# Kernel optimization log

Hardware: AMD Instinct MI355X
Metric: run time of the kernel (lower is better)

The kernel has to match this reference:

```python
import jax, jax.numpy as jnp
import numpy as np

NUM_HEADS = 8
DIM_HEAD = 40
SCALE = DIM_HEAD ** (-1.0 / 4.0)  # applied to q AND k, net 1/sqrt(dim_head)


def setup_inputs() -> dict:
    key = jax.random.key(0)
    ks = jax.random.split(key, 7)
    B, T, Dq = 16, 4096, 320
    S, Dc = 77, 768
    inner = NUM_HEADS * DIM_HEAD  # 320
    return {
        "x": jax.random.normal(ks[0], (B, T, Dq), jnp.float32),
        "context": jax.random.normal(ks[1], (B, S, Dc), jnp.float32),
        "Wq": jax.random.normal(ks[2], (Dq, inner), jnp.float32) * 0.02,
        "Wk": jax.random.normal(ks[3], (Dc, inner), jnp.float32) * 0.02,
        "Wv": jax.random.normal(ks[4], (Dc, inner), jnp.float32) * 0.02,
        "Wo": jax.random.normal(ks[5], (inner, Dq), jnp.float32) * 0.02,
        "bo": jnp.zeros((Dq,), jnp.float32),
    }


def reference(x, context, Wq, Wk, Wv, Wo, bo):
    B, T, _ = x.shape
    S = context.shape[1]
    H, C = NUM_HEADS, DIM_HEAD
    # projections; scale applied to q and k separately (dim_head^-1/4 each)
    q = (x @ Wq * SCALE).reshape(B, T, H, C)        # [B,T,H,C]
    k = (context @ Wk * SCALE).reshape(B, S, H, C)  # [B,S,H,C]
    v = (context @ Wv).reshape(B, S, H, C)          # [B,S,H,C]
    scores = jnp.einsum("bthc,bshc->bhts", q, k)    # [B,H,T,S]
    attn = jax.nn.softmax(scores, axis=-1)
    out = jnp.einsum("bhts,bshc->bthc", attn, v).reshape(B, T, H * C)
    return out @ Wo + bo
```

## Files before the change

kernel.cpp:

```cpp
#include <hip/hip_runtime.h>
#include <math.h>


#define NUM_HEADS 8
#define DIM_HEAD 40
#define INNER 320
#define DQ 320
#define DC 768
#define SEQ_T 4096
#define SEQ_S 77
#define BATCH 16
#define M_TOTAL (BATCH * SEQ_T)
#define MKV 1232
#define MKV_PAD 1280
#define SCALE 0.39763536438352531f

typedef __attribute__((ext_vector_type(8))) short short8;
typedef __attribute__((ext_vector_type(4))) float floatx4;

__device__ __forceinline__ unsigned short f2bf(float f) {
  unsigned u = __float_as_uint(f);
  u += 0x7FFFu + ((u >> 16) & 1u);
  return (unsigned short)(u >> 16);
}

#define CTXBLKS (MKV_PAD * DC / 8 / 256)
__global__ __launch_bounds__(256) void convert_ctx_kernel(
    const float* __restrict__ ctx, unsigned short* __restrict__ ctxb) {
  size_t t = (size_t)blockIdx.x * 256 + threadIdx.x;
  int row = (int)(t / (DC / 8)), col = (int)(t % (DC / 8)) * 8;
  int4 pk = make_int4(0, 0, 0, 0);
  if (row < MKV) {
    const float* p = &ctx[(size_t)row * DC + col];
    float4 a = *(const float4*)p, b = *(const float4*)(p + 4);
    pk.x = (int)(f2bf(a.x) | ((unsigned)f2bf(a.y) << 16));
    pk.y = (int)(f2bf(a.z) | ((unsigned)f2bf(a.w) << 16));
    pk.z = (int)(f2bf(b.x) | ((unsigned)f2bf(b.y) << 16));
    pk.w = (int)(f2bf(b.z) | ((unsigned)f2bf(b.w) << 16));
  }
  *(int4*)&ctxb[(size_t)row * DC + col] = pk;
}

__global__ __launch_bounds__(256) void transpose_w_kernel(
    const float* __restrict__ Wq, const float* __restrict__ Wo,
    const float* __restrict__ Wk, const float* __restrict__ Wv,
    unsigned short* __restrict__ WqT, unsigned short* __restrict__ WoT,
    unsigned short* __restrict__ WkvT) {
  const int z = blockIdx.z;
  const float* W; unsigned short* WT; int KD; float scl = 1.0f;
  if (z == 0)      { W = Wq; WT = WqT;  KD = 320; }
  else if (z == 1) { W = Wo; WT = WoT;  KD = 320; }
  else if (z == 2) { W = Wk; WT = WkvT; KD = DC; scl = SCALE; }
  else             { W = Wv; WT = WkvT + (size_t)INNER * DC; KD = DC; }
  const int k0 = blockIdx.x * 32;
  if (k0 >= KD) return;
  const int n0 = blockIdx.y * 32;
  __shared__ float tile[32][33];
  int tx = threadIdx.x & 31, ty = threadIdx.x >> 5;
  #pragma unroll
  for (int r = 0; r < 4; ++r)
    tile[ty + r * 8][tx] = W[(size_t)(k0 + ty + r * 8) * 320 + n0 + tx];
  __syncthreads();
  #pragma unroll
  for (int r = 0; r < 4; ++r)
    WT[(size_t)(n0 + ty + r * 8) * KD + k0 + tx] = f2bf(tile[tx][ty + r * 8] * scl);
}

#define GBM 128
#define GBN 160
#define GBK 64

template <bool OUT_BF16, int K, int CN>
__global__ __launch_bounds__(256) void gemm_mfma_kernel(
    const unsigned short* __restrict__ A, const unsigned short* __restrict__ B,
    void* __restrict__ C, const float* __restrict__ bias, float scale) {
  __shared__ __align__(16) unsigned short As[GBM * GBK];
  __shared__ __align__(16) unsigned short Bs[GBN * GBK];
  const int tid = threadIdx.x;
  const int lane = tid & 63, wave = tid >> 6;
  const int wm = (wave & 1) * 64, wn = (wave >> 1) * 80;
  const int lrow = lane & 15, quad = lane >> 4;
  const unsigned short* Ab = A + (size_t)blockIdx.x * GBM * K;
  const unsigned short* Bb = B + (size_t)blockIdx.y * GBN * K;

  floatx4 acc[4][5];
  #pragma unroll
  for (int i = 0; i < 4; ++i)
    #pragma unroll
    for (int j = 0; j < 5; ++j) acc[i][j] = (floatx4){0.f, 0.f, 0.f, 0.f};

  for (int kb = 0; kb < K / GBK; ++kb) {
    const int k0 = kb * GBK;
    #pragma unroll
    for (int rnd = 0; rnd < 4; ++rnd) {
      int off = rnd * 4096 + tid * 16;
      int m = off >> 7, cl = (off >> 4) & 7, cg = cl ^ (m & 7);
      __builtin_amdgcn_global_load_lds(
          (const __attribute__((address_space(1))) void*)(Ab + (size_t)m * K + k0 + cg * 8),
          (__attribute__((address_space(3))) void*)((char*)As + off), 16, 0, 0);
    }
    #pragma unroll
    for (int rnd = 0; rnd < 5; ++rnd) {
      int off = rnd * 4096 + tid * 16;
      int n = off >> 7, cl = (off >> 4) & 7, cg = cl ^ (n & 7);
      __builtin_amdgcn_global_load_lds(
          (const __attribute__((address_space(1))) void*)(Bb + (size_t)n * K + k0 + cg * 8),
          (__attribute__((address_space(3))) void*)((char*)Bs + off), 16, 0, 0);
    }
    __syncthreads();
    #pragma unroll
    for (int ks = 0; ks < 2; ++ks) {
      short8 fa[4], fb[5];
      #pragma unroll
      for (int i = 0; i < 4; ++i) {
        int m = wm + i * 16 + lrow;
        int cl = (ks * 4 + quad) ^ (m & 7);
        fa[i] = *(const short8*)&As[m * GBK + cl * 8];
      }
      #pragma unroll
      for (int j = 0; j < 5; ++j) {
        int n = wn + j * 16 + lrow;
        int cl = (ks * 4 + quad) ^ (n & 7);
        fb[j] = *(const short8*)&Bs[n * GBK + cl * 8];
      }
      #pragma unroll
      for (int i = 0; i < 4; ++i)
        #pragma unroll
        for (int j = 0; j < 5; ++j)
          acc[i][j] = __builtin_amdgcn_mfma_f32_16x16x32_bf16(fa[i], fb[j], acc[i][j], 0, 0, 0);
    }
    __syncthreads();
  }
  #pragma unroll
  for (int i = 0; i < 4; ++i)
    #pragma unroll
    for (int j = 0; j < 5; ++j) {
      int n = blockIdx.y * GBN + wn + j * 16 + lrow;
      float bv = bias ? bias[n] : 0.f;
      #pragma unroll
      for (int r = 0; r < 4; ++r) {
        size_t m = (size_t)blockIdx.x * GBM + wm + i * 16 + quad * 4 + r;
        float val = acc[i][j][r] * scale + bv;
        if (OUT_BF16) ((unsigned short*)C)[m * CN + n] = f2bf(val);
        else          ((float*)C)[m * CN + n] = val;
      }
    }
}

template <bool OUT_BF16, bool A_FP32>
__global__ __launch_bounds__(256, 2) void gemm_wide_kernel(
    const void* __restrict__ Av, const unsigned short* __restrict__ B,
    void* __restrict__ C, const float* __restrict__ bias, float scale) {
  __shared__ __align__(16) unsigned short As[128 * 64];
  __shared__ __align__(16) unsigned short Bs[320 * 64];
  const int tid = threadIdx.x;
  const int lane = tid & 63, wave = tid >> 6;
  const int wm = (wave & 1) * 64, wn = (wave >> 1) * 160;
  const int lrow = lane & 15, quad = lane >> 4;

  floatx4 acc[4][10];
  #pragma unroll
  for (int i = 0; i < 4; ++i)
    #pragma unroll
    for (int j = 0; j < 10; ++j) acc[i][j] = (floatx4){0.f, 0.f, 0.f, 0.f};

  for (int kb = 0; kb < 5; ++kb) {
    const int k0 = kb * 64;
    if (A_FP32) {
      const float* Af = (const float*)Av + (size_t)blockIdx.x * 128 * 320;
      #pragma unroll
      for (int rnd = 0; rnd < 4; ++rnd) {
        int off = rnd * 4096 + tid * 16;
        int m = off >> 7, cl = (off >> 4) & 7, cg = cl ^ (m & 7);
        const float* src = Af + (size_t)m * 320 + k0 + cg * 8;
        float4 a = *(const float4*)src, b = *(const float4*)(src + 4);
        short8 pk;
        pk[0] = (short)f2bf(a.x); pk[1] = (short)f2bf(a.y);
        pk[2] = (short)f2bf(a.z); pk[3] = (short)f2bf(a.w);
        pk[4] = (short)f2bf(b.x); pk[5] = (short)f2bf(b.y);
        pk[6] = (short)f2bf(b.z); pk[7] = (short)f2bf(b.w);
        *(short8*)((char*)As + off) = pk;
      }
    } else {
      const unsigned short* Ab = (const unsigned short*)Av + (size_t)blockIdx.x * 128 * 320;
      #pragma unroll
      for (int rnd = 0; rnd < 4; ++rnd) {
        int off = rnd * 4096 + tid * 16;
        int m = off >> 7, cl = (off >> 4) & 7, cg = cl ^ (m & 7);
        __builtin_amdgcn_global_load_lds(
            (const __attribute__((address_space(1))) void*)(Ab + (size_t)m * 320 + k0 + cg * 8),
            (__attribute__((address_space(3))) void*)((char*)As + off), 16, 0, 0);
      }
    }
    #pragma unroll
    for (int rnd = 0; rnd < 10; ++rnd) {
      int off = rnd * 4096 + tid * 16;
      int n = off >> 7, cl = (off >> 4) & 7, cg = cl ^ (n & 7);
      __builtin_amdgcn_global_load_lds(
          (const __attribute__((address_space(1))) void*)(B + (size_t)n * 320 + k0 + cg * 8),
          (__attribute__((address_space(3))) void*)((char*)Bs + off), 16, 0, 0);
    }
    __syncthreads();
    #pragma unroll
    for (int ks = 0; ks < 2; ++ks) {
      short8 fa[4], fb[10];
      #pragma unroll
      for (int i = 0; i < 4; ++i) {
        int m = wm + i * 16 + lrow;
        int cl = (ks * 4 + quad) ^ (m & 7);
        fa[i] = *(const short8*)&As[m * 64 + cl * 8];
      }
      #pragma unroll
      for (int j = 0; j < 10; ++j) {
        int n = wn + j * 16 + lrow;
        int cl = (ks * 4 + quad) ^ (n & 7);
        fb[j] = *(const short8*)&Bs[n * 64 + cl * 8];
      }
      #pragma unroll
      for (int i = 0; i < 4; ++i)
        #pragma unroll
        for (int j = 0; j < 10; ++j)
          acc[i][j] = __builtin_amdgcn_mfma_f32_16x16x32_bf16(fa[i], fb[j], acc[i][j], 0, 0, 0);
    }
    __syncthreads();
  }
  #pragma unroll
  for (int i = 0; i < 4; ++i)
    #pragma unroll
    for (int j = 0; j < 10; ++j) {
      int n = wn + j * 16 + lrow;
      float bv = bias ? bias[n] : 0.f;
      #pragma unroll
      for (int r = 0; r < 4; ++r) {
        size_t m = (size_t)blockIdx.x * 128 + wm + i * 16 + quad * 4 + r;
        float val = acc[i][j][r] * scale + bv;
        if (OUT_BF16) ((unsigned short*)C)[m * 320 + n] = f2bf(val);
        else          ((float*)C)[m * 320 + n] = val;
      }
    }
}

__global__ __launch_bounds__(256) void attn_mfma_kernel(
    const unsigned short* __restrict__ q, const float* __restrict__ kv,
    unsigned short* __restrict__ o) {
  __shared__ __align__(16) unsigned short lds[24064];
  unsigned short* Kb = lds;
  unsigned short* Vt = lds + 5760;
  unsigned short* Qb = lds + 10752;
  const int tid = threadIdx.x;
  const int lane = tid & 63, wave = tid >> 6;
  const int lrow = lane & 15, quad = lane >> 4;
  unsigned short* Pw = lds + 10752 + wave * 3328;
  const int b = blockIdx.x >> 3, h = blockIdx.x & 7;
  const int t0 = blockIdx.y * 128;
  const unsigned short* qblk = q + ((size_t)b * SEQ_T + t0) * INNER + h * DIM_HEAD;

  #pragma unroll
  for (int rnd = 0; rnd < 3; ++rnd) {
    int off = rnd * 4096 + tid * 16;
    if (off < 10240) {
      int row = off / 80, rb = off % 80;
      __builtin_amdgcn_global_load_lds(
          (const __attribute__((address_space(1))) void*)(qblk + (size_t)row * INNER + rb / 2),
          (__attribute__((address_space(3))) void*)((char*)Qb + off), 16, 0, 0);
    }
  }
  {
    int4 z = make_int4(0, 0, 0, 0);
    for (int i = tid; i < 1344; i += 256) ((int4*)lds)[i] = z;
  }
  __syncthreads();

  const float* kvb = kv + (size_t)b * SEQ_S * 640;
  for (int idx = tid; idx < SEQ_S * 10; idx += 256) {
    int s = idx / 10, c4 = (idx % 10) * 4;
    float4 kx = *(const float4*)&kvb[s * 640 + h * DIM_HEAD + c4];
    float4 vx = *(const float4*)&kvb[s * 640 + 320 + h * DIM_HEAD + c4];
    *(ushort4*)&Kb[s * 72 + c4] =
        make_ushort4(f2bf(kx.x), f2bf(kx.y), f2bf(kx.z), f2bf(kx.w));
    Vt[(c4 + 0) * 104 + s] = f2bf(vx.x);
    Vt[(c4 + 1) * 104 + s] = f2bf(vx.y);
    Vt[(c4 + 2) * 104 + s] = f2bf(vx.z);
    Vt[(c4 + 3) * 104 + s] = f2bf(vx.w);
  }
  __syncthreads();

  short8 fa[2][2];
  const short8 zero8 = {0, 0, 0, 0, 0, 0, 0, 0};
  #pragma unroll
  for (int i = 0; i < 2; ++i) {
    int row = wave * 32 + i * 16 + lrow;
    fa[i][0] = *(const short8*)&Qb[row * 40 + quad * 8];
    fa[i][1] = (quad == 0) ? *(const short8*)&Qb[row * 40 + 32] : zero8;
  }
  __syncthreads();

  floatx4 sc[2][5];
  #pragma unroll
  for (int i = 0; i < 2; ++i)
    #pragma unroll
    for (int j = 0; j < 5; ++j) sc[i][j] = (floatx4){0.f, 0.f, 0.f, 0.f};
  #pragma unroll
  for (int j = 0; j < 5; ++j) {
    int srow = j * 16 + lrow;
    short8 fb0 = *(const short8*)&Kb[srow * 72 + quad * 8];
    short8 fb1 = *(const short8*)&Kb[srow * 72 + 32 + quad * 8];
    #pragma unroll
    for (int i = 0; i < 2; ++i) {
      sc[i][j] = __builtin_amdgcn_mfma_f32_16x16x32_bf16(fa[i][0], fb0, sc[i][j], 0, 0, 0);
      sc[i][j] = __builtin_amdgcn_mfma_f32_16x16x32_bf16(fa[i][1], fb1, sc[i][j], 0, 0, 0);
    }
  }

  float lsum[2][4];
  #pragma unroll
  for (int i = 0; i < 2; ++i)
    #pragma unroll
    for (int r = 0; r < 4; ++r) lsum[i][r] = 0.f;
  #pragma unroll
  for (int i = 0; i < 2; ++i) {
    #pragma unroll
    for (int j = 0; j < 5; ++j) {
      int s = j * 16 + lrow;
      #pragma unroll
      for (int r = 0; r < 4; ++r) {
        float p = (s < SEQ_S) ? __expf(sc[i][j][r]) : 0.f;
        Pw[(i * 16 + quad * 4 + r) * 104 + s] = f2bf(p);
        lsum[i][r] += p;
      }
    }
    #pragma unroll
    for (int r = 0; r < 4; ++r)
      Pw[(i * 16 + quad * 4 + r) * 104 + 80 + lrow] = 0;
  }
  #pragma unroll
  for (int i = 0; i < 2; ++i)
    #pragma unroll
    for (int r = 0; r < 4; ++r) {
      float v = lsum[i][r];
      v += __shfl_xor(v, 1); v += __shfl_xor(v, 2);
      v += __shfl_xor(v, 4); v += __shfl_xor(v, 8);
      lsum[i][r] = 1.0f / v;
    }

  floatx4 oc[2][3];
  #pragma unroll
  for (int i = 0; i < 2; ++i)
    #pragma unroll
    for (int nj = 0; nj < 3; ++nj) oc[i][nj] = (floatx4){0.f, 0.f, 0.f, 0.f};
  #pragma unroll
  for (int ks = 0; ks < 3; ++ks) {
    short8 pa[2];
    #pragma unroll
    for (int i = 0; i < 2; ++i)
      pa[i] = *(const short8*)&Pw[(i * 16 + lrow) * 104 + ks * 32 + quad * 8];
    #pragma unroll
    for (int nj = 0; nj < 3; ++nj) {
      short8 vb = *(const short8*)&Vt[(nj * 16 + lrow) * 104 + ks * 32 + quad * 8];
      #pragma unroll
      for (int i = 0; i < 2; ++i)
        oc[i][nj] = __builtin_amdgcn_mfma_f32_16x16x32_bf16(pa[i], vb, oc[i][nj], 0, 0, 0);
    }
  }

  __syncthreads();
  unsigned short* Ost = lds;
  #pragma unroll
  for (int i = 0; i < 2; ++i)
    #pragma unroll
    for (int nj = 0; nj < 3; ++nj) {
      int c = nj * 16 + lrow;
      if (c < DIM_HEAD) {
        #pragma unroll
        for (int r = 0; r < 4; ++r) {
          int row = wave * 32 + i * 16 + quad * 4 + r;
          Ost[row * 40 + c] = f2bf(oc[i][nj][r] * lsum[i][r]);
        }
      }
    }
  __syncthreads();
  unsigned short* oblk = o + ((size_t)b * SEQ_T + t0) * INNER + h * DIM_HEAD;
  for (int u = tid; u < 640; u += 256) {
    int row = u / 5, c8 = (u % 5) * 8;
    *(int4*)(oblk + (size_t)row * INNER + c8) = *(const int4*)&Ost[u * 8];
  }
}

extern "C" void kernel_launch(void* const* d_in, const int* in_sizes, int n_in,
                              void* d_out, int out_size, void* d_ws, size_t ws_size,
                              hipStream_t stream) {
  const float* x   = (const float*)d_in[0];
  const float* ctx = (const float*)d_in[1];
  const float* Wq  = (const float*)d_in[2];
  const float* Wk  = (const float*)d_in[3];
  const float* Wv  = (const float*)d_in[4];
  const float* Wo  = (const float*)d_in[5];
  const float* bo  = (const float*)d_in[6];
  float* out = (float*)d_out;

  char* w = (char*)d_ws;
  unsigned short* qo   = (unsigned short*)(w);
  unsigned short* ctxb = (unsigned short*)(w + 41943040);
  unsigned short* WkvT = (unsigned short*)(w + 43909120);
  float*          kvw  = (float*)(w + 44892160);
  unsigned short* WqT  = (unsigned short*)(w + 48168960);
  unsigned short* WoT  = (unsigned short*)(w + 48373760);

  hipLaunchKernelGGL(convert_ctx_kernel, dim3(CTXBLKS), dim3(256), 0, stream, ctx, ctxb);
  hipLaunchKernelGGL(transpose_w_kernel, dim3(24, 10, 4), dim3(256), 0, stream,
                     Wq, Wo, Wk, Wv, WqT, WoT, WkvT);
  hipLaunchKernelGGL((gemm_mfma_kernel<false, DC, 640>), dim3(MKV_PAD / GBM, 640 / GBN),
                     dim3(256), 0, stream, ctxb, WkvT, (void*)kvw, (const float*)nullptr, 1.0f);
  hipLaunchKernelGGL((gemm_wide_kernel<true, true>), dim3(M_TOTAL / 128), dim3(256), 0,
                     stream, (const void*)x, WqT, (void*)qo, (const float*)nullptr, SCALE);
  hipLaunchKernelGGL(attn_mfma_kernel, dim3(BATCH * NUM_HEADS, SEQ_T / 128), dim3(256), 0,
                     stream, qo, kvw, qo);
  hipLaunchKernelGGL((gemm_wide_kernel<false, false>), dim3(M_TOTAL / 128), dim3(256), 0,
                     stream, (const void*)qo, WoT, (void*)out, bo, 1.0f);
}
```

Measured before the change: 269.2 us.

## Fuse Q projection, attention and output projection into one kernel

Replaces the separate Q GEMM, attention kernel and output GEMM with a single 512-thread kernel per 128-row tile. The tile computes Q into LDS, loops over all 8 heads doing attention with K/V pre-converted to bf16 by a new prep kernel, and writes the result back into the same LDS buffer before running the Wo GEMM. This removes the bf16 Q and attention-output round trips through global memory and two launches. In exchange the kernel needs about 138KB of LDS, which limits it to one block per CU, and it serialises per-head syncs with fewer waves in flight.

Result: faster. 255.6 us (-5.1%).

```diff
diff --git a/kernel.cpp b/kernel.cpp
--- a/kernel.cpp
+++ b/kernel.cpp
@@ -147,242 +147,234 @@
     }
 }
 
-template <bool OUT_BF16, bool A_FP32>
-__global__ __launch_bounds__(256, 2) void gemm_wide_kernel(
-    const void* __restrict__ Av, const unsigned short* __restrict__ B,
-    void* __restrict__ C, const float* __restrict__ bias, float scale) {
-  __shared__ __align__(16) unsigned short As[128 * 64];
-  __shared__ __align__(16) unsigned short Bs[320 * 64];
+__global__ __launch_bounds__(256) void prep_kv_kernel(
+    const float* __restrict__ kvw, unsigned short* __restrict__ kvp) {
+  const int b = blockIdx.x >> 3, h = blockIdx.x & 7;
+  unsigned short* dst = kvp + (size_t)blockIdx.x * 8192;
+  const float* kvb = kvw + (size_t)b * SEQ_S * 640;
+  for (int i = threadIdx.x; i < 3200; i += 256) {
+    int s = i / 40, c = i % 40;
+    unsigned short v = 0;
+    if (s < SEQ_S) v = f2bf(kvb[(size_t)s * 640 + h * DIM_HEAD + c]);
+    dst[i] = v;
+  }
+  for (int i = threadIdx.x; i < 4992; i += 256) {
+    int c = i / 104, s = i % 104;
+    unsigned short v = 0;
+    if (s < SEQ_S && c < DIM_HEAD)
+      v = f2bf(kvb[(size_t)s * 640 + 320 + h * DIM_HEAD + c]);
+    dst[3200 + i] = v;
+  }
+}
+
+#define QS_STRIDE 328
+#define LDS_STAGE 41984
+
+__global__ __launch_bounds__(512) void fused_attn_kernel(
+    const float* __restrict__ x, const unsigned short* __restrict__ WqT,
+    const unsigned short* __restrict__ kvp, const unsigned short* __restrict__ WoT,
+    const float* __restrict__ bo, float* __restrict__ out) {
+  __shared__ __align__(16) unsigned short lds[70656];
+  unsigned short* qs = lds;
+  unsigned short* As = lds + LDS_STAGE;
+  unsigned short* Bs = lds + LDS_STAGE + 8192;
   const int tid = threadIdx.x;
   const int lane = tid & 63, wave = tid >> 6;
-  const int wm = (wave & 1) * 64, wn = (wave >> 1) * 160;
   const int lrow = lane & 15, quad = lane >> 4;
-
-  floatx4 acc[4][10];
-  #pragma unroll
-  for (int i = 0; i < 4; ++i)
-    #pragma unroll
-    for (int j = 0; j < 10; ++j) acc[i][j] = (floatx4){0.f, 0.f, 0.f, 0.f};
-
-  for (int kb = 0; kb < 5; ++kb) {
-    const int k0 = kb * 64;
-    if (A_FP32) {
-      const float* Af = (const float*)Av + (size_t)blockIdx.x * 128 * 320;
-      #pragma unroll
-      for (int rnd = 0; rnd < 4; ++rnd) {
-        int off = rnd * 4096 + tid * 16;
+  const int b = blockIdx.x >> 5;
+  const int t0 = (blockIdx.x & 31) * 128;
+  const int wm = (wave & 1) * 64, wn = (wave >> 1) * 80;
+
+  {
+    const float* xb = x + ((size_t)b * SEQ_T + t0) * DQ;
+    floatx4 acc[4][5];
+    #pragma unroll
+    for (int i = 0; i < 4; ++i)
+      #pragma unroll
+      for (int j = 0; j < 5; ++j) acc[i][j] = (floatx4){0.f, 0.f, 0.f, 0.f};
+    for (int kb = 0; kb < 5; ++kb) {
+      const int k0 = kb * 64;
+      #pragma unroll
+      for (int rnd = 0; rnd < 2; ++rnd) {
+        int off = rnd * 8192 + tid * 16;
         int m = off >> 7, cl = (off >> 4) & 7, cg = cl ^ (m & 7);
-        const float* src = Af + (size_t)m * 320 + k0 + cg * 8;
-        float4 a = *(const float4*)src, b = *(const float4*)(src + 4);
+        const float* src = xb + (size_t)m * DQ + k0 + cg * 8;
+        float4 a = *(const float4*)src, c = *(const float4*)(src + 4);
         short8 pk;
         pk[0] = (short)f2bf(a.x); pk[1] = (short)f2bf(a.y);
         pk[2] = (short)f2bf(a.z); pk[3] = (short)f2bf(a.w);
-        pk[4] = (short)f2bf(b.x); pk[5] = (short)f2bf(b.y);
-        pk[6] = (short)f2bf(b.z); pk[7] = (short)f2bf(b.w);
+        pk[4] = (short)f2bf(c.x); pk[5] = (short)f2bf(c.y);
+        pk[6] = (short)f2bf(c.z); pk[7] = (short)f2bf(c.w);
         *(short8*)((char*)As + off) = pk;
       }
-    } else {
-      const unsigned short* Ab = (const unsigned short*)Av + (size_t)blockIdx.x * 128 * 320;
-      #pragma unroll
-      for (int rnd = 0; rnd < 4; ++rnd) {
-        int off = rnd * 4096 + tid * 16;
-        int m = off >> 7, cl = (off >> 4) & 7, cg = cl ^ (m & 7);
+      #pragma unroll
+      for (int rnd = 0; rnd < 5; ++rnd) {
+        int off = rnd * 8192 + tid * 16;
+        int n = off >> 7, cl = (off >> 4) & 7, cg = cl ^ (n & 7);
         __builtin_amdgcn_global_load_lds(
-            (const __attribute__((address_space(1))) void*)(Ab + (size_t)m * 320 + k0 + cg * 8),
-            (__attribute__((address_space(3))) void*)((char*)As + off), 16, 0, 0);
-      }
-    }
-    #pragma unroll
-    for (int rnd = 0; rnd < 10; ++rnd) {
-      int off = rnd * 4096 + tid * 16;
-      int n = off >> 7, cl = (off >> 4) & 7, cg = cl ^ (n & 7);
-      __builtin_amdgcn_global_load_lds(
-          (const __attribute__((address_space(1))) void*)(B + (size_t)n * 320 + k0 + cg * 8),
-          (__attribute__((address_space(3))) void*)((char*)Bs + off), 16, 0, 0);
-    }
-    __syncthreads();
-    #pragma unroll
-    for (int ks = 0; ks < 2; ++ks) {
-      short8 fa[4], fb[10];
-      #pragma unroll
-      for (int i = 0; i < 4; ++i) {
-        int m = wm + i * 16 + lrow;
-        int cl = (ks * 4 + quad) ^ (m & 7);
-        fa[i] = *(const short8*)&As[m * 64 + cl * 8];
-      }
-      #pragma unroll
-      for (int j = 0; j < 10; ++j) {
+            (const __attribute__((address_space(1))) void*)(WqT + (size_t)n * 320 + k0 + cg * 8),
+            (__attribute__((address_space(3))) void*)((char*)Bs + off), 16, 0, 0);
+      }
+      __syncthreads();
+      #pragma unroll
+      for (int ks = 0; ks < 2; ++ks) {
+        short8 fa[4], fb[5];
+        #pragma unroll
+        for (int i = 0; i < 4; ++i) {
+          int m = wm + i * 16 + lrow;
+          int cl = (ks * 4 + quad) ^ (m & 7);
+          fa[i] = *(const short8*)&As[m * 64 + cl * 8];
+        }
+        #pragma unroll
+        for (int j = 0; j < 5; ++j) {
+          int n = wn + j * 16 + lrow;
+          int cl = (ks * 4 + quad) ^ (n & 7);
+          fb[j] = *(const short8*)&Bs[n * 64 + cl * 8];
+        }
+        #pragma unroll
+        for (int i = 0; i < 4; ++i)
+          #pragma unroll
+          for (int j = 0; j < 5; ++j)
+            acc[i][j] = __builtin_amdgcn_mfma_f32_16x16x32_bf16(fa[i], fb[j], acc[i][j], 0, 0, 0);
+      }
+      __syncthreads();
+    }
+    #pragma unroll
+    for (int i = 0; i < 4; ++i)
+      #pragma unroll
+      for (int j = 0; j < 5; ++j)
+        #pragma unroll
+        for (int r = 0; r < 4; ++r)
+          qs[(wm + i * 16 + quad * 4 + r) * QS_STRIDE + wn + j * 16 + lrow] =
+              f2bf(acc[i][j][r] * SCALE);
+  }
+  __syncthreads();
+
+  {
+    unsigned short* Kb = lds + LDS_STAGE;
+    unsigned short* Vt = lds + LDS_STAGE + 3200;
+    unsigned short* Pw = lds + LDS_STAGE + 8192 + wave * 1664;
+    const short8 zero8 = {0, 0, 0, 0, 0, 0, 0, 0};
+    for (int h = 0; h < NUM_HEADS; ++h) {
+      const unsigned short* kvbh = kvp + (size_t)(b * NUM_HEADS + h) * 8192;
+      #pragma unroll
+      for (int rnd = 0; rnd < 2; ++rnd) {
+        int off = rnd * 8192 + tid * 16;
+        __builtin_amdgcn_global_load_lds(
+            (const __attribute__((address_space(1))) void*)((const char*)kvbh + off),
+            (__attribute__((address_space(3))) void*)((char*)Kb + off), 16, 0, 0);
+      }
+      __syncthreads();
+      const int qrow = wave * 16 + lrow;
+      short8 fq0 = *(const short8*)&qs[qrow * QS_STRIDE + h * DIM_HEAD + quad * 8];
+      short8 fq1 = (quad == 0)
+                       ? *(const short8*)&qs[qrow * QS_STRIDE + h * DIM_HEAD + 32]
+                       : zero8;
+      floatx4 sc[5];
+      #pragma unroll
+      for (int j = 0; j < 5; ++j) sc[j] = (floatx4){0.f, 0.f, 0.f, 0.f};
+      #pragma unroll
+      for (int j = 0; j < 5; ++j) {
+        int srow = j * 16 + lrow;
+        short8 fb0 = *(const short8*)&Kb[srow * 40 + quad * 8];
+        short8 fb1 = *(const short8*)&Kb[srow * 40 + 32 + quad * 8];
+        sc[j] = __builtin_amdgcn_mfma_f32_16x16x32_bf16(fq0, fb0, sc[j], 0, 0, 0);
+        sc[j] = __builtin_amdgcn_mfma_f32_16x16x32_bf16(fq1, fb1, sc[j], 0, 0, 0);
+      }
+      float lsum[4] = {0.f, 0.f, 0.f, 0.f};
+      #pragma unroll
+      for (int j = 0; j < 5; ++j) {
+        int s = j * 16 + lrow;
+        #pragma unroll
+        for (int r = 0; r < 4; ++r) {
+          float p = (s < SEQ_S) ? __expf(sc[j][r]) : 0.f;
+          Pw[(quad * 4 + r) * 104 + s] = f2bf(p);
+          lsum[r] += p;
+        }
+      }
+      #pragma unroll
+      for (int r = 0; r < 4; ++r) Pw[(quad * 4 + r) * 104 + 80 + lrow] = 0;
+      #pragma unroll
+      for (int r = 0; r < 4; ++r) {
+        float v = lsum[r];
+        v += __shfl_xor(v, 1); v += __shfl_xor(v, 2);
+        v += __shfl_xor(v, 4); v += __shfl_xor(v, 8);
+        lsum[r] = 1.0f / v;
+      }
+      floatx4 oc[3];
+      #pragma unroll
+      for (int nj = 0; nj < 3; ++nj) oc[nj] = (floatx4){0.f, 0.f, 0.f, 0.f};
+      #pragma unroll
+      for (int ks = 0; ks < 3; ++ks) {
+        short8 pa = *(const short8*)&Pw[lrow * 104 + ks * 32 + quad * 8];
+        #pragma unroll
+        for (int nj = 0; nj < 3; ++nj) {
+          short8 vb = *(const short8*)&Vt[(nj * 16 + lrow) * 104 + ks * 32 + quad * 8];
+          oc[nj] = __builtin_amdgcn_mfma_f32_16x16x32_bf16(pa, vb, oc[nj], 0, 0, 0);
+        }
+      }
+      #pragma unroll
+      for (int nj = 0; nj < 3; ++nj) {
+        int c = nj * 16 + lrow;
+        if (c < DIM_HEAD) {
+          #pragma unroll
+          for (int r = 0; r < 4; ++r)
+            qs[(wave * 16 + quad * 4 + r) * QS_STRIDE + h * DIM_HEAD + c] =
+                f2bf(oc[nj][r] * lsum[r]);
+        }
+      }
+      __syncthreads();
+    }
+  }
+
+  {
+    floatx4 acc[4][5];
+    #pragma unroll
+    for (int i = 0; i < 4; ++i)
+      #pragma unroll
+      for (int j = 0; j < 5; ++j) acc[i][j] = (floatx4){0.f, 0.f, 0.f, 0.f};
+    for (int kb = 0; kb < 5; ++kb) {
+      const int k0 = kb * 64;
+      #pragma unroll
+      for (int rnd = 0; rnd < 5; ++rnd) {
+        int off = rnd * 8192 + tid * 16;
+        int n = off >> 7, cl = (off >> 4) & 7, cg = cl ^ (n & 7);
+        __builtin_amdgcn_global_load_lds(
+            (const __attribute__((address_space(1))) void*)(WoT + (size_t)n * 320 + k0 + cg * 8),
+            (__attribute__((address_space(3))) void*)((char*)Bs + off), 16, 0, 0);
+      }
+      __syncthreads();
+      #pragma unroll
+      for (int ks = 0; ks < 2; ++ks) {
+        short8 fa[4], fb[5];
+        #pragma unroll
+        for (int i = 0; i < 4; ++i)
+          fa[i] = *(const short8*)&qs[(wm + i * 16 + lrow) * QS_STRIDE + k0 + ks * 32 + quad * 8];
+        #pragma unroll
+        for (int j = 0; j < 5; ++j) {
+          int n = wn + j * 16 + lrow;
+          int cl = (ks * 4 + quad) ^ (n & 7);
+          fb[j] = *(const short8*)&Bs[n * 64 + cl * 8];
+        }
+        #pragma unroll
+        for (int i = 0; i < 4; ++i)
+          #pragma unroll
+          for (int j = 0; j < 5; ++j)
+            acc[i][j] = __builtin_amdgcn_mfma_f32_16x16x32_bf16(fa[i], fb[j], acc[i][j], 0, 0, 0);
+      }
+      __syncthreads();
+    }
+    float* ob = out + ((size_t)b * SEQ_T + t0) * DQ;
+    #pragma unroll
+    for (int i = 0; i < 4; ++i)
+      #pragma unroll
+      for (int j = 0; j < 5; ++j) {
         int n = wn + j * 16 + lrow;
-        int cl = (ks * 4 + quad) ^ (n & 7);
-        fb[j] = *(const short8*)&Bs[n * 64 + cl * 8];
-      }
-      #pragma unroll
-      for (int i = 0; i < 4; ++i)
-        #pragma unroll
-        for (int j = 0; j < 10; ++j)
-          acc[i][j] = __builtin_amdgcn_mfma_f32_16x16x32_bf16(fa[i], fb[j], acc[i][j], 0, 0, 0);
-    }
-    __syncthreads();
-  }
-  #pragma unroll
-  for (int i = 0; i < 4; ++i)
-    #pragma unroll
-    for (int j = 0; j < 10; ++j) {
-      int n = wn + j * 16 + lrow;
-      float bv = bias ? bias[n] : 0.f;
-      #pragma unroll
-      for (int r = 0; r < 4; ++r) {
-        size_t m = (size_t)blockIdx.x * 128 + wm + i * 16 + quad * 4 + r;
-        float val = acc[i][j][r] * scale + bv;
-        if (OUT_BF16) ((unsigned short*)C)[m * 320 + n] = f2bf(val);
-        else          ((float*)C)[m * 320 + n] = val;
-      }
-    }
-}
-
-__global__ __launch_bounds__(256) void attn_mfma_kernel(
-    const unsigned short* __restrict__ q, const float* __restrict__ kv,
-    unsigned short* __restrict__ o) {
-  __shared__ __align__(16) unsigned short lds[24064];
-  unsigned short* Kb = lds;
-  unsigned short* Vt = lds + 5760;
-  unsigned short* Qb = lds + 10752;
-  const int tid = threadIdx.x;
-  const int lane = tid & 63, wave = tid >> 6;
-  const int lrow = lane & 15, quad = lane >> 4;
-  unsigned short* Pw = lds + 10752 + wave * 3328;
-  const int b = blockIdx.x >> 3, h = blockIdx.x & 7;
-  const int t0 = blockIdx.y * 128;
-  const unsigned short* qblk = q + ((size_t)b * SEQ_T + t0) * INNER + h * DIM_HEAD;
-
-  #pragma unroll
-  for (int rnd = 0; rnd < 3; ++rnd) {
-    int off = rnd * 4096 + tid * 16;
-    if (off < 10240) {
-      int row = off / 80, rb = off % 80;
-      __builtin_amdgcn_global_load_lds(
-          (const __attribute__((address_space(1))) void*)(qblk + (size_t)row * INNER + rb / 2),
-          (__attribute__((address_space(3))) void*)((char*)Qb + off), 16, 0, 0);
-    }
-  }
-  {
-    int4 z = make_int4(0, 0, 0, 0);
-    for (int i = tid; i < 1344; i += 256) ((int4*)lds)[i] = z;
-  }
-  __syncthreads();
-
-  const float* kvb = kv + (size_t)b * SEQ_S * 640;
-  for (int idx = tid; idx < SEQ_S * 10; idx += 256) {
-    int s = idx / 10, c4 = (idx % 10) * 4;
-    float4 kx = *(const float4*)&kvb[s * 640 + h * DIM_HEAD + c4];
-    float4 vx = *(const float4*)&kvb[s * 640 + 320 + h * DIM_HEAD + c4];
-    *(ushort4*)&Kb[s * 72 + c4] =
-        make_ushort4(f2bf(kx.x), f2bf(kx.y), f2bf(kx.z), f2bf(kx.w));
-    Vt[(c4 + 0) * 104 + s] = f2bf(vx.x);
-    Vt[(c4 + 1) * 104 + s] = f2bf(vx.y);
-    Vt[(c4 + 2) * 104 + s] = f2bf(vx.z);
-    Vt[(c4 + 3) * 104 + s] = f2bf(vx.w);
-  }
-  __syncthreads();
-
-  short8 fa[2][2];
-  const short8 zero8 = {0, 0, 0, 0, 0, 0, 0, 0};
-  #pragma unroll
-  for (int i = 0; i < 2; ++i) {
-    int row = wave * 32 + i * 16 + lrow;
-    fa[i][0] = *(const short8*)&Qb[row * 40 + quad * 8];
-    fa[i][1] = (quad == 0) ? *(const short8*)&Qb[row * 40 + 32] : zero8;
-  }
-  __syncthreads();
-
-  floatx4 sc[2][5];
-  #pragma unroll
-  for (int i = 0; i < 2; ++i)
-    #pragma unroll
-    for (int j = 0; j < 5; ++j) sc[i][j] = (floatx4){0.f, 0.f, 0.f, 0.f};
-  #pragma unroll
-  for (int j = 0; j < 5; ++j) {
-    int srow = j * 16 + lrow;
-    short8 fb0 = *(const short8*)&Kb[srow * 72 + quad * 8];
-    short8 fb1 = *(const short8*)&Kb[srow * 72 + 32 + quad * 8];
-    #pragma unroll
-    for (int i = 0; i < 2; ++i) {
-      sc[i][j] = __builtin_amdgcn_mfma_f32_16x16x32_bf16(fa[i][0], fb0, sc[i][j], 0, 0, 0);
-      sc[i][j] = __builtin_amdgcn_mfma_f32_16x16x32_bf16(fa[i][1], fb1, sc[i][j], 0, 0, 0);
-    }
-  }
-
-  float lsum[2][4];
-  #pragma unroll
-  for (int i = 0; i < 2; ++i)
-    #pragma unroll
-    for (int r = 0; r < 4; ++r) lsum[i][r] = 0.f;
-  #pragma unroll
-  for (int i = 0; i < 2; ++i) {
-    #pragma unroll
-    for (int j = 0; j < 5; ++j) {
-      int s = j * 16 + lrow;
-      #pragma unroll
-      for (int r = 0; r < 4; ++r) {
-        float p = (s < SEQ_S) ? __expf(sc[i][j][r]) : 0.f;
-        Pw[(i * 16 + quad * 4 + r) * 104 + s] = f2bf(p);
-        lsum[i][r] += p;
-      }
-    }
-    #pragma unroll
-    for (int r = 0; r < 4; ++r)
-      Pw[(i * 16 + quad * 4 + r) * 104 + 80 + lrow] = 0;
-  }
-  #pragma unroll
-  for (int i = 0; i < 2; ++i)
-    #pragma unroll
-    for (int r = 0; r < 4; ++r) {
-      float v = lsum[i][r];
-      v += __shfl_xor(v, 1); v += __shfl_xor(v, 2);
-      v += __shfl_xor(v, 4); v += __shfl_xor(v, 8);
-      lsum[i][r] = 1.0f / v;
-    }
-
-  floatx4 oc[2][3];
-  #pragma unroll
-  for (int i = 0; i < 2; ++i)
-    #pragma unroll
-    for (int nj = 0; nj < 3; ++nj) oc[i][nj] = (floatx4){0.f, 0.f, 0.f, 0.f};
-  #pragma unroll
-  for (int ks = 0; ks < 3; ++ks) {
-    short8 pa[2];
-    #pragma unroll
-    for (int i = 0; i < 2; ++i)
-      pa[i] = *(const short8*)&Pw[(i * 16 + lrow) * 104 + ks * 32 + quad * 8];
-    #pragma unroll
-    for (int nj = 0; nj < 3; ++nj) {
-      short8 vb = *(const short8*)&Vt[(nj * 16 + lrow) * 104 + ks * 32 + quad * 8];
-      #pragma unroll
-      for (int i = 0; i < 2; ++i)
-        oc[i][nj] = __builtin_amdgcn_mfma_f32_16x16x32_bf16(pa[i], vb, oc[i][nj], 0, 0, 0);
-    }
-  }
-
-  __syncthreads();
-  unsigned short* Ost = lds;
-  #pragma unroll
-  for (int i = 0; i < 2; ++i)
-    #pragma unroll
-    for (int nj = 0; nj < 3; ++nj) {
-      int c = nj * 16 + lrow;
-      if (c < DIM_HEAD) {
-        #pragma unroll
-        for (int r = 0; r < 4; ++r) {
-          int row = wave * 32 + i * 16 + quad * 4 + r;
-          Ost[row * 40 + c] = f2bf(oc[i][nj][r] * lsum[i][r]);
-        }
-      }
-    }
-  __syncthreads();
-  unsigned short* oblk = o + ((size_t)b * SEQ_T + t0) * INNER + h * DIM_HEAD;
-  for (int u = tid; u < 640; u += 256) {
-    int row = u / 5, c8 = (u % 5) * 8;
-    *(int4*)(oblk + (size_t)row * INNER + c8) = *(const int4*)&Ost[u * 8];
+        float bv = bo[n];
+        #pragma unroll
+        for (int r = 0; r < 4; ++r)
+          ob[(size_t)(wm + i * 16 + quad * 4 + r) * DQ + n] = acc[i][j][r] + bv;
+      }
   }
 }
 
@@ -399,22 +391,19 @@
   float* out = (float*)d_out;
 
   char* w = (char*)d_ws;
-  unsigned short* qo   = (unsigned short*)(w);
-  unsigned short* ctxb = (unsigned short*)(w + 41943040);
-  unsigned short* WkvT = (unsigned short*)(w + 43909120);
-  float*          kvw  = (float*)(w + 44892160);
-  unsigned short* WqT  = (unsigned short*)(w + 48168960);
-  unsigned short* WoT  = (unsigned short*)(w + 48373760);
+  unsigned short* ctxb = (unsigned short*)(w);
+  unsigned short* WkvT = (unsigned short*)(w + 1966080);
+  float*          kvw  = (float*)(w + 2949120);
+  unsigned short* WqT  = (unsigned short*)(w + 6225920);
+  unsigned short* WoT  = (unsigned short*)(w + 6430720);
+  unsigned short* kvp  = (unsigned short*)(w + 6635520);
 
   hipLaunchKernelGGL(convert_ctx_kernel, dim3(CTXBLKS), dim3(256), 0, stream, ctx, ctxb);
   hipLaunchKernelGGL(transpose_w_kernel, dim3(24, 10, 4), dim3(256), 0, stream,
                      Wq, Wo, Wk, Wv, WqT, WoT, WkvT);
   hipLaunchKernelGGL((gemm_mfma_kernel<false, DC, 640>), dim3(MKV_PAD / GBM, 640 / GBN),
                      dim3(256), 0, stream, ctxb, WkvT, (void*)kvw, (const float*)nullptr, 1.0f);
-  hipLaunchKernelGGL((gemm_wide_kernel<true, true>), dim3(M_TOTAL / 128), dim3(256), 0,
-                     stream, (const void*)x, WqT, (void*)qo, (const float*)nullptr, SCALE);
-  hipLaunchKernelGGL(attn_mfma_kernel, dim3(BATCH * NUM_HEADS, SEQ_T / 128), dim3(256), 0,
-                     stream, qo, kvw, qo);
-  hipLaunchKernelGGL((gemm_wide_kernel<false, false>), dim3(M_TOTAL / 128), dim3(256), 0,
-                     stream, (const void*)qo, WoT, (void*)out, bo, 1.0f);
-}
+  hipLaunchKernelGGL(prep_kv_kernel, dim3(BATCH * NUM_HEADS), dim3(256), 0, stream, kvw, kvp);
+  hipLaunchKernelGGL(fused_attn_kernel, dim3(BATCH * (SEQ_T / 128)), dim3(512), 0, stream,
+                     x, WqT, kvp, WoT, bo, out);
+}
```
